# Performance work log

Hardware: AMD Instinct MI355X
Metric: run time of the kernel (lower is better)

## Reference

```python
import jax, jax.numpy as jnp
import numpy as np

MAX_AGENTS = 64
IN_DIM = 256
HID_DIM = 512
OUT_DIM = 256
MAX_CHILDREN = 8
BATCH = 1024


def setup_inputs() -> dict:
    key = jax.random.key(0)
    k1, k2, k3, k4, k5 = jax.random.split(key, 5)
    W1 = jax.random.normal(k1, (MAX_AGENTS, IN_DIM, HID_DIM), dtype=jnp.float32) * 0.02
    b1 = jnp.zeros((MAX_AGENTS, HID_DIM), dtype=jnp.float32)
    W2 = jax.random.normal(k2, (MAX_AGENTS, HID_DIM, OUT_DIM), dtype=jnp.float32) * 0.02
    b2 = jnp.zeros((MAX_AGENTS, OUT_DIM), dtype=jnp.float32)
    router_weights = jax.random.normal(k3, (MAX_AGENTS, HID_DIM, MAX_CHILDREN), dtype=jnp.float32) * 0.01
    agent_indices = jax.random.randint(k4, (BATCH,), 0, MAX_AGENTS, dtype=jnp.int64 if jax.config.jax_enable_x64 else jnp.int32)
    x = jax.random.normal(k5, (BATCH, IN_DIM), dtype=jnp.float32)
    return {
        "x": x,
        "W1": W1,
        "b1": b1,
        "W2": W2,
        "b2": b2,
        "router_weights": router_weights,
        "agent_indices": agent_indices,
    }


def reference(x, W1, b1, W2, b2, router_weights, agent_indices):
    # Gather per-sample weights (same as torch advanced indexing W1[agent_indices])
    w1 = W1[agent_indices]           # [B, In, Hid]
    b1g = b1[agent_indices]          # [B, Hid]
    w2 = W2[agent_indices]           # [B, Hid, Out]
    b2g = b2[agent_indices]          # [B, Out]
    rw = router_weights[agent_indices]  # [B, Hid, C]

    # per-sample MLP: bmm with a singleton row -> einsum
    h = jax.nn.relu(jnp.einsum('bi,bih->bh', x, w1) + b1g)      # [B, Hid]
    out = jnp.einsum('bh,bho->bo', h, w2) + b2g                 # [B, Out]
    r_logits = jnp.einsum('bh,bhc->bc', h, rw)                  # [B, C]
    return (h, out, r_logits)
```

## Files before the change

### kernel.cpp

```cpp
#include <hip/hip_runtime.h>

#define IN_DIM   256
#define HID_DIM  512
#define OUT_DIM  256
#define N_CHILD  8
#define BATCH    1024

#define SB    16
#define XPAD  20
#define MAXCH 128

extern "C" __global__ __launch_bounds__(1024)
void prep_sort(const int* __restrict__ raw, int* __restrict__ sorted,
               int* __restrict__ ch_agent, int* __restrict__ ch_start,
               int* __restrict__ ch_len, float* __restrict__ zdst)
{
    const int t = threadIdx.x;
    if (blockIdx.x > 0) {
        const int total4 = (BATCH * N_CHILD) / 4;
        const float4 z = make_float4(0.f, 0.f, 0.f, 0.f);
        for (int i = t; i < total4; i += 1024)
            ((float4*)zdst)[i] = z;
        return;
    }
    __shared__ int cnt[64], cnt2[64], start[64];
    __shared__ int is32, totch;
    if (t < 64) { cnt[t] = 0; cnt2[t] = 0; }
    if (t == 0) is32 = 0;
    __syncthreads();
    if (raw[2 * (t & 511) + 1] != 0) is32 = 1;
    __syncthreads();
    const int a = (is32 ? raw[t] : raw[2 * t]) & 63;
    atomicAdd(&cnt[a], 1);
    __syncthreads();
    if (t < 64) {
        const int c   = cnt[t];
        const int nch = (c + SB - 1) / SB;
        int sc = c, sn = nch;
        #pragma unroll
        for (int d = 1; d < 64; d <<= 1) {
            const int vc = __shfl_up(sc, d);
            const int vn = __shfl_up(sn, d);
            if (t >= d) { sc += vc; sn += vn; }
        }
        const int off = sc - c;
        start[t] = off;
        const int chb = sn - nch;
        for (int p = 0, j = 0; p < c; p += SB, ++j) {
            ch_agent[chb + j] = t;
            ch_start[chb + j] = off + p;
            ch_len[chb + j]   = (c - p < SB) ? (c - p) : SB;
        }
        if (t == 63) totch = sn;
    }
    __syncthreads();
    if (t >= totch && t < MAXCH) ch_len[t] = 0;
    const int pos = start[a] + atomicAdd(&cnt2[a], 1);
    sorted[pos] = t;
}

extern "C" __global__ __launch_bounds__(256)
void k1_mlp1(const float* __restrict__ x, const float* __restrict__ W1,
             const float* __restrict__ b1, const float* __restrict__ rw,
             const int* __restrict__ sorted, const int* __restrict__ ch_agent,
             const int* __restrict__ ch_start, const int* __restrict__ ch_len,
             float* __restrict__ h_out, float* __restrict__ r_out)
{
    const int chunk = blockIdx.x;
    const int len = ch_len[chunk];
    if (len == 0) return;
    const int a  = ch_agent[chunk];
    const int cs = ch_start[chunk];
    const int t  = threadIdx.x;
    const int bcol = blockIdx.y * 64;

    __shared__ float xT[IN_DIM * XPAD];
    __shared__ float wS[64 * 64];
    __shared__ int   sid[SB];

    if (t < SB) sid[t] = sorted[cs + (t < len ? t : len - 1)];
    __syncthreads();

    const float* Wb = W1 + (size_t)a * IN_DIM * HID_DIM + bcol;
    const int sr  = t >> 4;
    const int sc4 = (t & 15) * 4;
    #define WLD(P,I) (*(const float4*)(Wb + (size_t)((P)*64 + sr + (I)*16) * HID_DIM + sc4))

    float4 wr0 = WLD(0,0), wr1 = WLD(0,1), wr2 = WLD(0,2), wr3 = WLD(0,3);

    #pragma unroll
    for (int s = 0; s < SB; ++s)
        xT[t * XPAD + s] = x[(size_t)sid[s] * IN_DIM + t];

    const int cg = t & 15;
    const int kq = (t >> 4) & 3;
    const int w  = t >> 6;
    const bool act = (w * 4) < len;

    float acc[16];
    #pragma unroll
    for (int i = 0; i < 16; ++i) acc[i] = 0.f;

    for (int p = 0; p < IN_DIM / 64; ++p) {
        __syncthreads();
        *(float4*)(&wS[(sr +  0) * 64 + sc4]) = wr0;
        *(float4*)(&wS[(sr + 16) * 64 + sc4]) = wr1;
        *(float4*)(&wS[(sr + 32) * 64 + sc4]) = wr2;
        *(float4*)(&wS[(sr + 48) * 64 + sc4]) = wr3;
        __syncthreads();
        if (p < 3) {
            wr0 = WLD(p+1,0); wr1 = WLD(p+1,1);
            wr2 = WLD(p+1,2); wr3 = WLD(p+1,3);
        }
        if (act) {
            #pragma unroll
            for (int i = 0; i < 16; ++i) {
                const int row = i * 4 + kq;
                const float4 wv = *(const float4*)(&wS[row * 64 + cg * 4]);
                const float4 xv = *(const float4*)(&xT[(p * 64 + row) * XPAD + w * 4]);
                const float wa[4] = {wv.x, wv.y, wv.z, wv.w};
                const float xa[4] = {xv.x, xv.y, xv.z, xv.w};
                #pragma unroll
                for (int c = 0; c < 4; ++c)
                    #pragma unroll
                    for (int s = 0; s < 4; ++s)
                        acc[c * 4 + s] = fmaf(wa[c], xa[s], acc[c * 4 + s]);
            }
        }
    }
    #undef WLD

    if (!act) return;

    #pragma unroll
    for (int i = 0; i < 16; ++i) {
        acc[i] += __shfl_xor(acc[i], 16);
        acc[i] += __shfl_xor(acc[i], 32);
    }

    if (kq != 0) return;

    const float4 bv = *(const float4*)(b1 + a * HID_DIM + bcol + cg * 4);
    const float ba[4] = {bv.x, bv.y, bv.z, bv.w};
    float hv[16];
    #pragma unroll
    for (int c = 0; c < 4; ++c)
        #pragma unroll
        for (int s = 0; s < 4; ++s)
            hv[c * 4 + s] = fmaxf(acc[c * 4 + s] + ba[c], 0.f);

    #pragma unroll
    for (int s = 0; s < 4; ++s) {
        float4 v = make_float4(hv[0 * 4 + s], hv[1 * 4 + s],
                               hv[2 * 4 + s], hv[3 * 4 + s]);
        *(float4*)(h_out + (size_t)sid[w * 4 + s] * HID_DIM + bcol + cg * 4) = v;
    }

    float rp[32];
    #pragma unroll
    for (int i = 0; i < 32; ++i) rp[i] = 0.f;
    const float* rwa = rw + (size_t)a * HID_DIM * N_CHILD
                          + (size_t)(bcol + cg * 4) * N_CHILD;
    #pragma unroll
    for (int j = 0; j < 4; ++j)
        #pragma unroll
        for (int ch = 0; ch < 8; ++ch) {
            const float rv = rwa[j * N_CHILD + ch];
            #pragma unroll
            for (int s = 0; s < 4; ++s)
                rp[s * 8 + ch] = fmaf(hv[j * 4 + s], rv, rp[s * 8 + ch]);
        }
    #pragma unroll
    for (int i = 0; i < 32; ++i) {
        rp[i] += __shfl_xor(rp[i], 1);
        rp[i] += __shfl_xor(rp[i], 2);
        rp[i] += __shfl_xor(rp[i], 4);
        rp[i] += __shfl_xor(rp[i], 8);
    }
    if (cg == 0) {
        #pragma unroll
        for (int s = 0; s < 4; ++s) {
            const int sg = w * 4 + s;
            if (sg < len) {
                float* rdst = r_out + (size_t)sid[sg] * N_CHILD;
                #pragma unroll
                for (int ch = 0; ch < 8; ++ch)
                    atomicAdd(rdst + ch, rp[s * 8 + ch]);
            }
        }
    }
}

extern "C" __global__ __launch_bounds__(256)
void k2_mlp2(const float* __restrict__ h, const float* __restrict__ W2,
             const float* __restrict__ b2,
             const int* __restrict__ sorted, const int* __restrict__ ch_agent,
             const int* __restrict__ ch_start, const int* __restrict__ ch_len,
             float* __restrict__ o_out)
{
    const int chunk = blockIdx.x;
    const int len = ch_len[chunk];
    if (len == 0) return;
    const int a  = ch_agent[chunk];
    const int cs = ch_start[chunk];
    const int t  = threadIdx.x;
    const int bcol = blockIdx.y * 64;

    __shared__ float hT[64 * XPAD];
    __shared__ float wS[64 * 64];
    __shared__ int   sid[SB];

    if (t < SB) sid[t] = sorted[cs + (t < len ? t : len - 1)];
    __syncthreads();

    const float* Wb = W2 + (size_t)a * HID_DIM * OUT_DIM + bcol;
    const int sr   = t >> 4;
    const int sc4  = (t & 15) * 4;
    const int hrow = t & 63;
    const int hsb  = (t >> 6) * 4;
    #define WLD2(P,I) (*(const float4*)(Wb + (size_t)((P)*64 + sr + (I)*16) * OUT_DIM + sc4))
    #define HLD(P,J)  (h[(size_t)sid[hsb + (J)] * HID_DIM + (P)*64 + hrow])

    float4 wr0 = WLD2(0,0), wr1 = WLD2(0,1), wr2 = WLD2(0,2), wr3 = WLD2(0,3);
    float  hr0 = HLD(0,0),  hr1 = HLD(0,1),  hr2 = HLD(0,2),  hr3 = HLD(0,3);

    const int cg = t & 15;
    const int kq = (t >> 4) & 3;
    const int w  = t >> 6;
    const bool act = (w * 4) < len;

    float acc[16];
    #pragma unroll
    for (int i = 0; i < 16; ++i) acc[i] = 0.f;

    for (int p = 0; p < HID_DIM / 64; ++p) {
        __syncthreads();
        hT[hrow * XPAD + hsb + 0] = hr0;
        hT[hrow * XPAD + hsb + 1] = hr1;
        hT[hrow * XPAD + hsb + 2] = hr2;
        hT[hrow * XPAD + hsb + 3] = hr3;
        *(float4*)(&wS[(sr +  0) * 64 + sc4]) = wr0;
        *(float4*)(&wS[(sr + 16) * 64 + sc4]) = wr1;
        *(float4*)(&wS[(sr + 32) * 64 + sc4]) = wr2;
        *(float4*)(&wS[(sr + 48) * 64 + sc4]) = wr3;
        __syncthreads();
        if (p < 7) {
            wr0 = WLD2(p+1,0); wr1 = WLD2(p+1,1);
            wr2 = WLD2(p+1,2); wr3 = WLD2(p+1,3);
            hr0 = HLD(p+1,0);  hr1 = HLD(p+1,1);
            hr2 = HLD(p+1,2);  hr3 = HLD(p+1,3);
        }
        if (act) {
            #pragma unroll
            for (int i = 0; i < 16; ++i) {
                const int row = i * 4 + kq;
                const float4 wv = *(const float4*)(&wS[row * 64 + cg * 4]);
                const float4 xv = *(const float4*)(&hT[row * XPAD + w * 4]);
                const float wa[4] = {wv.x, wv.y, wv.z, wv.w};
                const float xa[4] = {xv.x, xv.y, xv.z, xv.w};
                #pragma unroll
                for (int c = 0; c < 4; ++c)
                    #pragma unroll
                    for (int s = 0; s < 4; ++s)
                        acc[c * 4 + s] = fmaf(wa[c], xa[s], acc[c * 4 + s]);
            }
        }
    }
    #undef WLD2
    #undef HLD

    if (!act) return;
    #pragma unroll
    for (int i = 0; i < 16; ++i) {
        acc[i] += __shfl_xor(acc[i], 16);
        acc[i] += __shfl_xor(acc[i], 32);
    }
    if (kq == 0) {
        const float4 bv = *(const float4*)(b2 + a * OUT_DIM + bcol + cg * 4);
        #pragma unroll
        for (int s = 0; s < 4; ++s) {
            const int g = w * 4 + s;
            if (g < len) {
                float4 v = make_float4(acc[0 * 4 + s] + bv.x,
                                       acc[1 * 4 + s] + bv.y,
                                       acc[2 * 4 + s] + bv.z,
                                       acc[3 * 4 + s] + bv.w);
                *(float4*)(o_out + (size_t)sid[g] * OUT_DIM + bcol + cg * 4) = v;
            }
        }
    }
}

extern "C" void kernel_launch(void* const* d_in, const int* in_sizes, int n_in,
                              void* d_out, int out_size, void* d_ws, size_t ws_size,
                              hipStream_t stream) {
    const float* x  = (const float*)d_in[0];
    const float* W1 = (const float*)d_in[1];
    const float* b1 = (const float*)d_in[2];
    const float* W2 = (const float*)d_in[3];
    const float* b2 = (const float*)d_in[4];
    const float* rw = (const float*)d_in[5];
    const int* raw  = (const int*)d_in[6];

    int* ws       = (int*)d_ws;
    int* sorted   = ws;
    int* ch_agent = ws + 1024;
    int* ch_start = ws + 1152;
    int* ch_len   = ws + 1280;

    float* out   = (float*)d_out;
    float* h_out = out;
    float* o_out = h_out + (size_t)BATCH * HID_DIM;
    float* r_out = o_out + (size_t)BATCH * OUT_DIM;

    hipLaunchKernelGGL(prep_sort, dim3(2), dim3(1024), 0, stream,
                       raw, sorted, ch_agent, ch_start, ch_len, r_out);
    hipLaunchKernelGGL(k1_mlp1, dim3(MAXCH, 8), dim3(256), 0, stream,
                       x, W1, b1, rw, sorted, ch_agent, ch_start, ch_len,
                       h_out, r_out);
    hipLaunchKernelGGL(k2_mlp2, dim3(MAXCH, 4), dim3(256), 0, stream,
                       h_out, W2, b2, sorted, ch_agent, ch_start, ch_len, o_out);
}
```

Baseline: 130.9 us.

## Fuse agent sort into MLP kernels and replace router atomics with partial-sum reduction

Removes the separate prep_sort launch: each block of both MLP kernels recomputes the per-agent histogram and its own chunk's sample list in shared memory. Router logits are now written as per-column-tile partial sums to workspace and reduced in the second kernel, which removes the atomics and the zeroing pass. The second kernel also uses 32-wide output tiles with a grid of 8 along y, doubling its block count. The cost is redundant sorting work in every block and an extra partial-sum buffer read.

```diff
diff --git a/kernel.cpp b/kernel.cpp
--- a/kernel.cpp
+++ b/kernel.cpp
@@ -10,76 +10,90 @@
 #define XPAD  20
 #define MAXCH 128
 
-extern "C" __global__ __launch_bounds__(1024)
-void prep_sort(const int* __restrict__ raw, int* __restrict__ sorted,
-               int* __restrict__ ch_agent, int* __restrict__ ch_start,
-               int* __restrict__ ch_len, float* __restrict__ zdst)
+__device__ __forceinline__ int sort_chunk(const int* __restrict__ raw, const int c,
+                                          int* s_cnt, int* s_info, int* s_wsum,
+                                          int* s_sid)
 {
     const int t = threadIdx.x;
-    if (blockIdx.x > 0) {
-        const int total4 = (BATCH * N_CHILD) / 4;
-        const float4 z = make_float4(0.f, 0.f, 0.f, 0.f);
-        for (int i = t; i < total4; i += 1024)
-            ((float4*)zdst)[i] = z;
-        return;
-    }
-    __shared__ int cnt[64], cnt2[64], start[64];
-    __shared__ int is32, totch;
-    if (t < 64) { cnt[t] = 0; cnt2[t] = 0; }
-    if (t == 0) is32 = 0;
-    __syncthreads();
-    if (raw[2 * (t & 511) + 1] != 0) is32 = 1;
-    __syncthreads();
-    const int a = (is32 ? raw[t] : raw[2 * t]) & 63;
-    atomicAdd(&cnt[a], 1);
+    const int lane = t & 63, w = t >> 6;
+    if (t < 64) s_cnt[t] = 0;
+    if (t == 0) { s_info[2] = 0; s_info[3] = 0; }
+    __syncthreads();
+    if (raw[2 * t + 1] != 0 || raw[2 * (t + 256) + 1] != 0) s_info[3] = 1;
+    __syncthreads();
+    const int is32 = s_info[3];
+    int myid[4];
+    #pragma unroll
+    for (int j = 0; j < 4; ++j) {
+        const int i = t * 4 + j;
+        const int v = (is32 ? raw[i] : raw[2 * i]) & 63;
+        myid[j] = v;
+        atomicAdd(&s_cnt[v], 1);
+    }
     __syncthreads();
     if (t < 64) {
-        const int c   = cnt[t];
-        const int nch = (c + SB - 1) / SB;
-        int sc = c, sn = nch;
+        const int ca  = s_cnt[t];
+        const int nch = (ca + SB - 1) / SB;
+        int sn = nch;
         #pragma unroll
         for (int d = 1; d < 64; d <<= 1) {
-            const int vc = __shfl_up(sc, d);
-            const int vn = __shfl_up(sn, d);
-            if (t >= d) { sc += vc; sn += vn; }
-        }
-        const int off = sc - c;
-        start[t] = off;
+            const int v = __shfl_up(sn, d);
+            if (lane >= d) sn += v;
+        }
         const int chb = sn - nch;
-        for (int p = 0, j = 0; p < c; p += SB, ++j) {
-            ch_agent[chb + j] = t;
-            ch_start[chb + j] = off + p;
-            ch_len[chb + j]   = (c - p < SB) ? (c - p) : SB;
-        }
-        if (t == 63) totch = sn;
-    }
-    __syncthreads();
-    if (t >= totch && t < MAXCH) ch_len[t] = 0;
-    const int pos = start[a] + atomicAdd(&cnt2[a], 1);
-    sorted[pos] = t;
+        if (c >= chb && c < chb + nch) {
+            s_info[0] = t;
+            const int p = (c - chb) * SB;
+            s_info[1] = p;
+            s_info[2] = (ca - p < SB) ? (ca - p) : SB;
+        }
+    }
+    __syncthreads();
+    const int len = s_info[2];
+    if (len == 0) return 0;
+    const int a = s_info[0], p = s_info[1];
+    int m = 0;
+    #pragma unroll
+    for (int j = 0; j < 4; ++j) if (myid[j] == a) ++m;
+    int inc = m;
+    #pragma unroll
+    for (int d = 1; d < 64; d <<= 1) {
+        const int v = __shfl_up(inc, d);
+        if (lane >= d) inc += v;
+    }
+    if (lane == 63) s_wsum[w] = inc;
+    __syncthreads();
+    int base = inc - m;
+    #pragma unroll
+    for (int ww = 0; ww < 4; ++ww) if (ww < w) base += s_wsum[ww];
+    #pragma unroll
+    for (int j = 0; j < 4; ++j)
+        if (myid[j] == a) {
+            const int r = (base++) - p;
+            if (r >= 0 && r < SB) s_sid[r] = t * 4 + j;
+        }
+    __syncthreads();
+    if (t >= len && t < SB) s_sid[t] = s_sid[len - 1];
+    __syncthreads();
+    return len;
 }
 
 extern "C" __global__ __launch_bounds__(256)
 void k1_mlp1(const float* __restrict__ x, const float* __restrict__ W1,
              const float* __restrict__ b1, const float* __restrict__ rw,
-             const int* __restrict__ sorted, const int* __restrict__ ch_agent,
-             const int* __restrict__ ch_start, const int* __restrict__ ch_len,
-             float* __restrict__ h_out, float* __restrict__ r_out)
+             const int* __restrict__ raw,
+             float* __restrict__ h_out, float* __restrict__ r_part)
 {
-    const int chunk = blockIdx.x;
-    const int len = ch_len[chunk];
-    if (len == 0) return;
-    const int a  = ch_agent[chunk];
-    const int cs = ch_start[chunk];
-    const int t  = threadIdx.x;
-    const int bcol = blockIdx.y * 64;
-
     __shared__ float xT[IN_DIM * XPAD];
     __shared__ float wS[64 * 64];
-    __shared__ int   sid[SB];
-
-    if (t < SB) sid[t] = sorted[cs + (t < len ? t : len - 1)];
-    __syncthreads();
+    __shared__ int s_cnt[64], s_info[4], s_wsum[4], s_sid[SB];
+
+    const int chunk = blockIdx.x;
+    const int t = threadIdx.x;
+    const int len = sort_chunk(raw, chunk, s_cnt, s_info, s_wsum, s_sid);
+    if (len == 0) return;
+    const int a    = s_info[0];
+    const int bcol = blockIdx.y * 64;
 
     const float* Wb = W1 + (size_t)a * IN_DIM * HID_DIM + bcol;
     const int sr  = t >> 4;
@@ -90,7 +104,7 @@
 
     #pragma unroll
     for (int s = 0; s < SB; ++s)
-        xT[t * XPAD + s] = x[(size_t)sid[s] * IN_DIM + t];
+        xT[t * XPAD + s] = x[(size_t)s_sid[s] * IN_DIM + t];
 
     const int cg = t & 15;
     const int kq = (t >> 4) & 3;
@@ -131,13 +145,11 @@
     #undef WLD
 
     if (!act) return;
-
     #pragma unroll
     for (int i = 0; i < 16; ++i) {
         acc[i] += __shfl_xor(acc[i], 16);
         acc[i] += __shfl_xor(acc[i], 32);
     }
-
     if (kq != 0) return;
 
     const float4 bv = *(const float4*)(b1 + a * HID_DIM + bcol + cg * 4);
@@ -153,7 +165,7 @@
     for (int s = 0; s < 4; ++s) {
         float4 v = make_float4(hv[0 * 4 + s], hv[1 * 4 + s],
                                hv[2 * 4 + s], hv[3 * 4 + s]);
-        *(float4*)(h_out + (size_t)sid[w * 4 + s] * HID_DIM + bcol + cg * 4) = v;
+        *(float4*)(h_out + (size_t)s_sid[w * 4 + s] * HID_DIM + bcol + cg * 4) = v;
     }
 
     float rp[32];
@@ -178,54 +190,44 @@
         rp[i] += __shfl_xor(rp[i], 8);
     }
     if (cg == 0) {
-        #pragma unroll
-        for (int s = 0; s < 4; ++s) {
-            const int sg = w * 4 + s;
-            if (sg < len) {
-                float* rdst = r_out + (size_t)sid[sg] * N_CHILD;
-                #pragma unroll
-                for (int ch = 0; ch < 8; ++ch)
-                    atomicAdd(rdst + ch, rp[s * 8 + ch]);
-            }
-        }
+        float* rb = r_part + ((size_t)chunk * 8 + blockIdx.y) * 128 + w * 32;
+        #pragma unroll
+        for (int s4 = 0; s4 < 8; ++s4)
+            *(float4*)(rb + s4 * 4) = make_float4(rp[s4*4+0], rp[s4*4+1],
+                                                  rp[s4*4+2], rp[s4*4+3]);
     }
 }
 
 extern "C" __global__ __launch_bounds__(256)
 void k2_mlp2(const float* __restrict__ h, const float* __restrict__ W2,
-             const float* __restrict__ b2,
-             const int* __restrict__ sorted, const int* __restrict__ ch_agent,
-             const int* __restrict__ ch_start, const int* __restrict__ ch_len,
-             float* __restrict__ o_out)
+             const float* __restrict__ b2, const int* __restrict__ raw,
+             const float* __restrict__ r_part,
+             float* __restrict__ o_out, float* __restrict__ r_out)
 {
+    __shared__ float hT[64 * XPAD];
+    __shared__ float wS[64 * 32];
+    __shared__ int s_cnt[64], s_info[4], s_wsum[4], s_sid[SB];
+
     const int chunk = blockIdx.x;
-    const int len = ch_len[chunk];
+    const int t = threadIdx.x;
+    const int len = sort_chunk(raw, chunk, s_cnt, s_info, s_wsum, s_sid);
     if (len == 0) return;
-    const int a  = ch_agent[chunk];
-    const int cs = ch_start[chunk];
-    const int t  = threadIdx.x;
-    const int bcol = blockIdx.y * 64;
-
-    __shared__ float hT[64 * XPAD];
-    __shared__ float wS[64 * 64];
-    __shared__ int   sid[SB];
-
-    if (t < SB) sid[t] = sorted[cs + (t < len ? t : len - 1)];
-    __syncthreads();
+    const int a    = s_info[0];
+    const int bcol = blockIdx.y * 32;
 
     const float* Wb = W2 + (size_t)a * HID_DIM * OUT_DIM + bcol;
-    const int sr   = t >> 4;
-    const int sc4  = (t & 15) * 4;
+    const int r2   = t >> 3;
+    const int c4   = (t & 7) * 4;
     const int hrow = t & 63;
     const int hsb  = (t >> 6) * 4;
-    #define WLD2(P,I) (*(const float4*)(Wb + (size_t)((P)*64 + sr + (I)*16) * OUT_DIM + sc4))
-    #define HLD(P,J)  (h[(size_t)sid[hsb + (J)] * HID_DIM + (P)*64 + hrow])
-
-    float4 wr0 = WLD2(0,0), wr1 = WLD2(0,1), wr2 = WLD2(0,2), wr3 = WLD2(0,3);
-    float  hr0 = HLD(0,0),  hr1 = HLD(0,1),  hr2 = HLD(0,2),  hr3 = HLD(0,3);
-
-    const int cg = t & 15;
-    const int kq = (t >> 4) & 3;
+    #define WLD2(P,I) (*(const float4*)(Wb + (size_t)((P)*64 + r2 + (I)*32) * OUT_DIM + c4))
+    #define HLD(P,J)  (h[(size_t)s_sid[hsb + (J)] * HID_DIM + (P)*64 + hrow])
+
+    float4 wr0 = WLD2(0,0), wr1 = WLD2(0,1);
+    float  hr0 = HLD(0,0), hr1 = HLD(0,1), hr2 = HLD(0,2), hr3 = HLD(0,3);
+
+    const int cg = t & 7;
+    const int kq = (t >> 3) & 7;
     const int w  = t >> 6;
     const bool act = (w * 4) < len;
 
@@ -239,22 +241,19 @@
         hT[hrow * XPAD + hsb + 1] = hr1;
         hT[hrow * XPAD + hsb + 2] = hr2;
         hT[hrow * XPAD + hsb + 3] = hr3;
-        *(float4*)(&wS[(sr +  0) * 64 + sc4]) = wr0;
-        *(float4*)(&wS[(sr + 16) * 64 + sc4]) = wr1;
-        *(float4*)(&wS[(sr + 32) * 64 + sc4]) = wr2;
-        *(float4*)(&wS[(sr + 48) * 64 + sc4]) = wr3;
+        *(float4*)(&wS[(r2 +  0) * 32 + c4]) = wr0;
+        *(float4*)(&wS[(r2 + 32) * 32 + c4]) = wr1;
         __syncthreads();
         if (p < 7) {
             wr0 = WLD2(p+1,0); wr1 = WLD2(p+1,1);
-            wr2 = WLD2(p+1,2); wr3 = WLD2(p+1,3);
             hr0 = HLD(p+1,0);  hr1 = HLD(p+1,1);
             hr2 = HLD(p+1,2);  hr3 = HLD(p+1,3);
         }
         if (act) {
             #pragma unroll
-            for (int i = 0; i < 16; ++i) {
-                const int row = i * 4 + kq;
-                const float4 wv = *(const float4*)(&wS[row * 64 + cg * 4]);
+            for (int i = 0; i < 8; ++i) {
+                const int row = i * 8 + kq;
+                const float4 wv = *(const float4*)(&wS[row * 32 + cg * 4]);
                 const float4 xv = *(const float4*)(&hT[row * XPAD + w * 4]);
                 const float wa[4] = {wv.x, wv.y, wv.z, wv.w};
                 const float xa[4] = {xv.x, xv.y, xv.z, xv.w};
@@ -269,13 +268,13 @@
     #undef WLD2
     #undef HLD
 
-    if (!act) return;
     #pragma unroll
     for (int i = 0; i < 16; ++i) {
+        acc[i] += __shfl_xor(acc[i], 8);
         acc[i] += __shfl_xor(acc[i], 16);
         acc[i] += __shfl_xor(acc[i], 32);
     }
-    if (kq == 0) {
+    if (act && kq == 0) {
         const float4 bv = *(const float4*)(b2 + a * OUT_DIM + bcol + cg * 4);
         #pragma unroll
         for (int s = 0; s < 4; ++s) {
@@ -285,8 +284,18 @@
                                        acc[1 * 4 + s] + bv.y,
                                        acc[2 * 4 + s] + bv.z,
                                        acc[3 * 4 + s] + bv.w);
-                *(float4*)(o_out + (size_t)sid[g] * OUT_DIM + bcol + cg * 4) = v;
+                *(float4*)(o_out + (size_t)s_sid[g] * OUT_DIM + bcol + cg * 4) = v;
             }
+        }
+    }
+    if (blockIdx.y == 0 && t < 128) {
+        const int s = t >> 3;
+        if (s < len) {
+            float sum = 0.f;
+            #pragma unroll
+            for (int yy = 0; yy < 8; ++yy)
+                sum += r_part[((size_t)chunk * 8 + yy) * 128 + t];
+            r_out[(size_t)s_sid[s] * N_CHILD + (t & 7)] = sum;
         }
     }
 }
@@ -302,22 +311,15 @@
     const float* rw = (const float*)d_in[5];
     const int* raw  = (const int*)d_in[6];
 
-    int* ws       = (int*)d_ws;
-    int* sorted   = ws;
-    int* ch_agent = ws + 1024;
-    int* ch_start = ws + 1152;
-    int* ch_len   = ws + 1280;
+    float* r_part = (float*)d_ws;
 
     float* out   = (float*)d_out;
     float* h_out = out;
     float* o_out = h_out + (size_t)BATCH * HID_DIM;
     float* r_out = o_out + (size_t)BATCH * OUT_DIM;
 
-    hipLaunchKernelGGL(prep_sort, dim3(2), dim3(1024), 0, stream,
-                       raw, sorted, ch_agent, ch_start, ch_len, r_out);
     hipLaunchKernelGGL(k1_mlp1, dim3(MAXCH, 8), dim3(256), 0, stream,
-                       x, W1, b1, rw, sorted, ch_agent, ch_start, ch_len,
-                       h_out, r_out);
-    hipLaunchKernelGGL(k2_mlp2, dim3(MAXCH, 4), dim3(256), 0, stream,
-                       h_out, W2, b2, sorted, ch_agent, ch_start, ch_len, o_out);
+                       x, W1, b1, rw, raw, h_out, r_part);
+    hipLaunchKernelGGL(k2_mlp2, dim3(MAXCH, 8), dim3(256), 0, stream,
+                       h_out, W2, b2, raw, r_part, o_out, r_out);
 }
```

New measurement: 129.2 us, median of 2. No clear change (-1.3%).
